# Kernel tuning notes

Measured on AMD Instinct MI355X. Metric: run time of the kernel, lower is better.

The kernel has to match this reference:

```python
import jax, jax.numpy as jnp
import numpy as np

C = 512
H = 8
D = C // H
GROUPS = 32
EPS = 1e-5

def setup_inputs() -> dict:
    key = jax.random.key(0)
    ks = jax.random.split(key, 7)
    B, L = 4, 2048
    x = jax.random.normal(ks[0], (B, C, L), dtype=jnp.float32)
    gamma = jnp.ones((C,), dtype=jnp.float32)
    beta = jnp.zeros((C,), dtype=jnp.float32)
    w_qkv = jax.random.normal(ks[1], (3 * C, C), dtype=jnp.float32) * (1.0 / np.sqrt(C))
    b_qkv = jax.random.normal(ks[2], (3 * C,), dtype=jnp.float32) * 0.01
    w_proj = jax.random.normal(ks[3], (C, C), dtype=jnp.float32) * (1.0 / np.sqrt(C))
    b_proj = jax.random.normal(ks[4], (C,), dtype=jnp.float32) * 0.01
    return {"x": x, "gamma": gamma, "beta": beta, "w_qkv": w_qkv,
            "b_qkv": b_qkv, "w_proj": w_proj, "b_proj": b_proj}

def _group_norm(x, gamma, beta):
    B, Cc, L = x.shape
    xg = x.reshape(B, GROUPS, Cc // GROUPS, L)
    mean = jnp.mean(xg, axis=(2, 3), keepdims=True)
    var = jnp.var(xg, axis=(2, 3), keepdims=True)
    xn = ((xg - mean) * jax.lax.rsqrt(var + EPS)).reshape(B, Cc, L)
    return xn * gamma[None, :, None] + beta[None, :, None]

def reference(x, gamma, beta, w_qkv, b_qkv, w_proj, b_proj):
    B, Cc, L = x.shape
    h = _group_norm(x, gamma, beta)
    # 1x1 conv == channel matmul: (3C,C) x (B,C,L) -> (B,3C,L)
    qkv = jnp.einsum('oc,bcl->bol', w_qkv, h) + b_qkv[None, :, None]
    q, k, v = jnp.split(qkv, 3, axis=1)
    # (B,C,L) -> (B,H,L,D)
    def to_heads(t):
        return t.reshape(B, H, D, L).transpose(0, 1, 3, 2)
    q, k, v = to_heads(q), to_heads(k), to_heads(v)
    scale = 1.0 / np.sqrt(D).astype(np.float32)
    attn = jnp.einsum('bhqd,bhkd->bhqk', q, k) * scale  # [B,H,L,L]
    attn = jax.nn.softmax(attn, axis=-1)
    out = jnp.einsum('bhqk,bhkd->bhqd', attn, v)  # [B,H,L,D]
    out = out.transpose(0, 1, 3, 2).reshape(B, Cc, L)
    proj = jnp.einsum('oc,bcl->bol', w_proj, out) + b_proj[None, :, None]
    return x + proj
```

## Files before the change

kernel.cpp:

```cpp
#include <hip/hip_runtime.h>
#include <stdint.h>

#define C_DIM 512
#define H_HEADS 8
#define D_HEAD 64
#define B_BATCH 4
#define L_SEQ 2048
#define GROUPS 32
#define EPS_GN 1e-5f

typedef unsigned short u16;
typedef __attribute__((ext_vector_type(8))) __bf16 bf16x8;
typedef __attribute__((ext_vector_type(2))) float f32x2;
typedef __attribute__((ext_vector_type(4))) float f32x4;
typedef __attribute__((ext_vector_type(16))) float f32x16;

__device__ __forceinline__ u16 f2bf(float f) {
  unsigned u = __builtin_bit_cast(unsigned, f);
  unsigned r = u + 0x7FFFu + ((u >> 16) & 1u);
  return (u16)(r >> 16);
}

__device__ __forceinline__ unsigned cvtpk_bf16(float lo, float hi) {
  unsigned r;
  asm("v_cvt_pk_bf16_f32 %0, %1, %2" : "=v"(r) : "v"(lo), "v"(hi));
  return r;
}

__device__ __forceinline__ void pl32swap(unsigned& a, unsigned& b) {
  asm("v_permlane32_swap_b32 %0, %1" : "+v"(a), "+v"(b));
}

__device__ __forceinline__ bf16x8 mk8(unsigned a, unsigned b, unsigned c, unsigned d) {
  union { uint4 u; bf16x8 v; } z;
  z.u.x = a; z.u.y = b; z.u.z = c; z.u.w = d;
  return z.v;
}

__device__ __forceinline__ void gl16(const void* g, void* l) {
  __builtin_amdgcn_global_load_lds((const __attribute__((address_space(1))) void*)g,
                                   (__attribute__((address_space(3))) void*)l, 16, 0, 0);
}

__global__ __launch_bounds__(256) void cvt_weights(const float* __restrict__ wq,
                                                   const float* __restrict__ wp,
                                                   u16* __restrict__ wq_bf,
                                                   u16* __restrict__ wp_bf) {
  int i = blockIdx.x * 256 + threadIdx.x;
  const int nq = 3 * C_DIM * C_DIM;
  int idx = i * 4;
  const float* src;
  u16* dst;
  if (idx < nq) { src = wq + idx; dst = wq_bf + idx; }
  else          { src = wp + (idx - nq); dst = wp_bf + (idx - nq); }
  float4 v = *(const float4*)src;
  uint2 pk;
  pk.x = (unsigned)f2bf(v.x) | ((unsigned)f2bf(v.y) << 16);
  pk.y = (unsigned)f2bf(v.z) | ((unsigned)f2bf(v.w) << 16);
  *(uint2*)dst = pk;
}

__global__ __launch_bounds__(256) void groupnorm_kernel(const float* __restrict__ x,
                                                        const float* __restrict__ gamma,
                                                        const float* __restrict__ beta,
                                                        u16* __restrict__ h_t) {
  int bg = blockIdx.x;
  int b = bg >> 5, g = bg & 31;
  const float* base = x + ((size_t)(b * C_DIM + g * 16)) * L_SEQ;
  int t = threadIdx.x;
  int w = t >> 6;
  float s = 0.f, sq = 0.f;
  for (int i = 0; i < 32; ++i) {
    float4 v = ((const float4*)base)[t + i * 256];
    s += v.x + v.y + v.z + v.w;
    sq += v.x * v.x + v.y * v.y + v.z * v.z + v.w * v.w;
  }
  for (int off = 32; off; off >>= 1) { s += __shfl_down(s, off); sq += __shfl_down(sq, off); }
  __shared__ float red[8];
  if ((t & 63) == 0) { red[w * 2] = s; red[w * 2 + 1] = sq; }
  __syncthreads();
  float ts = red[0] + red[2] + red[4] + red[6];
  float tq = red[1] + red[3] + red[5] + red[7];
  float mean = ts * (1.f / 32768.f);
  float var = tq * (1.f / 32768.f) - mean * mean;
  float rstd = rsqrtf(var + EPS_GN);
  float ga[16], be[16];
#pragma unroll
  for (int c = 0; c < 16; ++c) {
    float gm = gamma[g * 16 + c];
    ga[c] = gm * rstd;
    be[c] = beta[g * 16 + c] - mean * gm * rstd;
  }
  __shared__ float tile[16][260];
  for (int lc = 0; lc < 8; ++lc) {
    __syncthreads();
#pragma unroll
    for (int it = 0; it < 4; ++it) {
      int r = it * 4 + w;
      int c4 = (t & 63) * 4;
      *(float4*)&tile[r][c4] = *(const float4*)(base + (size_t)r * L_SEQ + lc * 256 + c4);
    }
    __syncthreads();
    int l = lc * 256 + t;
    unsigned wds[8];
#pragma unroll
    for (int c = 0; c < 8; ++c) {
      float a0 = tile[2 * c][t] * ga[2 * c] + be[2 * c];
      float a1 = tile[2 * c + 1][t] * ga[2 * c + 1] + be[2 * c + 1];
      wds[c] = (unsigned)f2bf(a0) | ((unsigned)f2bf(a1) << 16);
    }
    u16* dst = h_t + ((size_t)(b * L_SEQ + l)) * C_DIM + g * 16;
    uint4 p0; p0.x = wds[0]; p0.y = wds[1]; p0.z = wds[2]; p0.w = wds[3];
    uint4 p1; p1.x = wds[4]; p1.y = wds[5]; p1.z = wds[6]; p1.w = wds[7];
    *(uint4*)dst = p0;
    *(uint4*)(dst + 8) = p1;
  }
}

template <int MODE>
__global__ __launch_bounds__(256) void gemm_kernel(const u16* __restrict__ A_bf,
                                                   const u16* __restrict__ B_t,
                                                   const float* __restrict__ bias,
                                                   const float* __restrict__ xres,
                                                   u16* __restrict__ q_t,
                                                   u16* __restrict__ kf_g,
                                                   u16* __restrict__ vf_g,
                                                   float* __restrict__ out_f) {
  constexpr int K = 512;
  __shared__ u16 A_lds[128][32];
  __shared__ u16 B_lds[128][32];
  int t = threadIdx.x;
  int w = t >> 6, lane = t & 63;
  int q4 = lane >> 4, c15 = lane & 15;
  int wm = w >> 1, wn = w & 1;
  int o0 = blockIdx.y * 128;
  int l0 = blockIdx.x * 128;
  int b = blockIdx.z;
  const u16* Bb = B_t + (size_t)b * L_SEQ * K;
  f32x4 acc[4][4] = {};

  int sr = lane >> 2, sc = lane & 3;
  int r0 = w * 32 + sr;
  int r1 = r0 + 16;
  int lc0 = (sc - (r0 >> 1)) & 3;
  int lc1 = (sc - (r1 >> 1)) & 3;
  const u16* Ag0 = A_bf + (size_t)(o0 + r0) * K + lc0 * 8;
  const u16* Ag1 = A_bf + (size_t)(o0 + r1) * K + lc1 * 8;
  const u16* Bg0 = Bb + (size_t)(l0 + r0) * K + lc0 * 8;
  const u16* Bg1 = Bb + (size_t)(l0 + r1) * K + lc1 * 8;
  u16* Al0 = &A_lds[w * 32][0];
  u16* Al1 = &A_lds[w * 32 + 16][0];
  u16* Bl0 = &B_lds[w * 32][0];
  u16* Bl1 = &B_lds[w * 32 + 16][0];

  for (int kt = 0; kt < K / 32; ++kt) {
    gl16(Ag0, Al0); gl16(Ag1, Al1);
    gl16(Bg0, Bl0); gl16(Bg1, Bl1);
    Ag0 += 32; Ag1 += 32; Bg0 += 32; Bg1 += 32;
    __syncthreads();
    bf16x8 af[4], bfr[4];
#pragma unroll
    for (int mi = 0; mi < 4; ++mi) {
      int ar = wm * 64 + mi * 16 + c15;
      af[mi] = *(const bf16x8*)&A_lds[ar][((q4 + (ar >> 1)) & 3) * 8];
    }
#pragma unroll
    for (int ni = 0; ni < 4; ++ni) {
      int br = wn * 64 + ni * 16 + c15;
      bfr[ni] = *(const bf16x8*)&B_lds[br][((q4 + (br >> 1)) & 3) * 8];
    }
#pragma unroll
    for (int mi = 0; mi < 4; ++mi)
#pragma unroll
      for (int ni = 0; ni < 4; ++ni)
        acc[mi][ni] = __builtin_amdgcn_mfma_f32_16x16x32_bf16(af[mi], bfr[ni], acc[mi][ni], 0, 0, 0);
    __syncthreads();
  }

  if (MODE == 0) {
    const float QS = 0.18033688f;
    int sel = o0 >> 9;
    int ob = o0 - sel * 512 + wm * 64;
#pragma unroll
    for (int mi = 0; mi < 4; ++mi) {
      int orow = ob + mi * 16 + q4 * 4;
      float4 bi = *(const float4*)&bias[o0 + wm * 64 + mi * 16 + q4 * 4];
#pragma unroll
      for (int ni = 0; ni < 4; ++ni) {
        int l = l0 + wn * 64 + ni * 16 + c15;
        float v0 = acc[mi][ni][0] + bi.x;
        float v1 = acc[mi][ni][1] + bi.y;
        float v2 = acc[mi][ni][2] + bi.z;
        float v3 = acc[mi][ni][3] + bi.w;
        if (sel == 0) {
          v0 *= QS; v1 *= QS; v2 *= QS; v3 *= QS;
          uint2 pk;
          pk.x = (unsigned)f2bf(v0) | ((unsigned)f2bf(v1) << 16);
          pk.y = (unsigned)f2bf(v2) | ((unsigned)f2bf(v3) << 16);
          *(uint2*)(q_t + ((size_t)(b * L_SEQ + l)) * C_DIM + orow) = pk;
        } else if (sel == 1) {
          int hh = orow >> 6, d = orow & 63;
          size_t base = ((size_t)(b * 8 + hh)) * 131072 +
                        (size_t)(((l >> 5) * 4 + (d >> 4))) * 512 +
                        (size_t)((l & 31) + ((d >> 3) & 1) * 32) * 8 + (d & 7);
          uint2 pk;
          pk.x = (unsigned)f2bf(v0) | ((unsigned)f2bf(v1) << 16);
          pk.y = (unsigned)f2bf(v2) | ((unsigned)f2bf(v3) << 16);
          *(uint2*)(kf_g + base) = pk;
        } else {
          int hh = orow >> 6, d = orow & 63;
          size_t base0 = ((size_t)(b * 8 + hh)) * 131072 +
                         (size_t)(l >> 4) * 1024 +
                         (size_t)((l >> 3) & 1) * 256 + (l & 7);
          vf_g[base0 + (size_t)((d + 0) >> 5) * 512 + ((d + 0) & 31) * 8] = f2bf(v0);
          vf_g[base0 + (size_t)((d + 1) >> 5) * 512 + ((d + 1) & 31) * 8] = f2bf(v1);
          vf_g[base0 + (size_t)((d + 2) >> 5) * 512 + ((d + 2) & 31) * 8] = f2bf(v2);
          vf_g[base0 + (size_t)((d + 3) >> 5) * 512 + ((d + 3) & 31) * 8] = f2bf(v3);
        }
      }
    }
  } else {
#pragma unroll
    for (int mi = 0; mi < 4; ++mi) {
      int orow = o0 + wm * 64 + mi * 16 + q4 * 4;
      float4 bi = *(const float4*)&bias[orow];
#pragma unroll
      for (int ni = 0; ni < 4; ++ni) {
        int l = l0 + wn * 64 + ni * 16 + c15;
        size_t base2 = ((size_t)(b * C_DIM + orow)) * L_SEQ + l;
        out_f[base2] = acc[mi][ni][0] + bi.x + xres[base2];
        out_f[base2 + L_SEQ] = acc[mi][ni][1] + bi.y + xres[base2 + L_SEQ];
        out_f[base2 + 2 * L_SEQ] = acc[mi][ni][2] + bi.z + xres[base2 + 2 * L_SEQ];
        out_f[base2 + 3 * L_SEQ] = acc[mi][ni][3] + bi.w + xres[base2 + 3 * L_SEQ];
      }
    }
  }
}

#define ATILE(KC, KN, T)                                                       \
  {                                                                            \
    int tn = (T) + 1; tn = tn > 15 ? 15 : tn;                                  \
    const u16* kp = kfb + tn * 2048;                                           \
    const u16* vp = vfb + (T) * 2048;                                          \
    KN[0] = *(const bf16x8*)(kp);                                              \
    KN[1] = *(const bf16x8*)(kp + 512);                                        \
    KN[2] = *(const bf16x8*)(kp + 1024);                                       \
    KN[3] = *(const bf16x8*)(kp + 1536);                                       \
    bf16x8 v0 = *(const bf16x8*)(vp);                                          \
    bf16x8 v1 = *(const bf16x8*)(vp + 512);                                    \
    bf16x8 v2 = *(const bf16x8*)(vp + 1024);                                   \
    bf16x8 v3 = *(const bf16x8*)(vp + 1536);                                   \
    f32x16 s;                                                                  \
    _Pragma("unroll") for (int r = 0; r < 16; ++r) s[r] = 0.f;                 \
    s = __builtin_amdgcn_mfma_f32_32x32x16_bf16(KC[0], qf[0], s, 0, 0, 0);     \
    s = __builtin_amdgcn_mfma_f32_32x32x16_bf16(KC[1], qf[1], s, 0, 0, 0);     \
    s = __builtin_amdgcn_mfma_f32_32x32x16_bf16(KC[2], qf[2], s, 0, 0, 0);     \
    s = __builtin_amdgcn_mfma_f32_32x32x16_bf16(KC[3], qf[3], s, 0, 0, 0);     \
    float mx = fmaxf(fmaxf(s[0], s[1]), s[2]);                                 \
    float m1_ = fmaxf(fmaxf(s[3], s[4]), s[5]);                                \
    float m2_ = fmaxf(fmaxf(s[6], s[7]), s[8]);                                \
    float m3_ = fmaxf(fmaxf(s[9], s[10]), s[11]);                              \
    float m4_ = fmaxf(fmaxf(s[12], s[13]), s[14]);                             \
    mx = fmaxf(fmaxf(mx, s[15]), fmaxf(m1_, m2_));                             \
    mx = fmaxf(mx, fmaxf(m3_, m4_));                                           \
    mx = fmaxf(mx, __shfl_xor(mx, 32));                                        \
    if (__any(mx > m_r + 8.f)) {                                               \
      float mnew = fmaxf(m_r, mx);                                             \
      float al = __builtin_amdgcn_exp2f(m_r - mnew);                           \
      l_r *= al;                                                               \
      _Pragma("unroll") for (int r = 0; r < 16; ++r) { o0[r] *= al; o1[r] *= al; } \
      m_r = mnew;                                                              \
    }                                                                          \
    _Pragma("unroll") for (int r = 0; r < 16; ++r)                             \
        s[r] = __builtin_amdgcn_exp2f(s[r] - m_r);                             \
    f32x2 a0_ = {s[0], s[1]}, a1_ = {s[2], s[3]}, a2_ = {s[4], s[5]},          \
          a3_ = {s[6], s[7]}, a4_ = {s[8], s[9]}, a5_ = {s[10], s[11]},        \
          a6_ = {s[12], s[13]}, a7_ = {s[14], s[15]};                          \
    f32x2 b0_ = a0_ + a1_, b1_ = a2_ + a3_, b2_ = a4_ + a5_, b3_ = a6_ + a7_;  \
    f32x2 c0_ = b0_ + b1_, c1_ = b2_ + b3_;                                    \
    f32x2 d0_ = c0_ + c1_;                                                     \
    float sum = d0_[0] + d0_[1];                                               \
    sum += __shfl_xor(sum, 32);                                                \
    l_r += sum;                                                                \
    unsigned pk[8];                                                            \
    _Pragma("unroll") for (int i = 0; i < 8; ++i)                              \
        pk[i] = cvtpk_bf16(s[2 * i], s[2 * i + 1]);                            \
    pl32swap(pk[0], pk[2]); pl32swap(pk[1], pk[3]);                            \
    pl32swap(pk[4], pk[6]); pl32swap(pk[5], pk[7]);                            \
    bf16x8 pf0 = mk8(pk[0], pk[1], pk[2], pk[3]);                              \
    bf16x8 pf1 = mk8(pk[4], pk[5], pk[6], pk[7]);                              \
    o0 = __builtin_amdgcn_mfma_f32_32x32x16_bf16(v0, pf0, o0, 0, 0, 0);        \
    o1 = __builtin_amdgcn_mfma_f32_32x32x16_bf16(v1, pf0, o1, 0, 0, 0);        \
    o0 = __builtin_amdgcn_mfma_f32_32x32x16_bf16(v2, pf1, o0, 0, 0, 0);        \
    o1 = __builtin_amdgcn_mfma_f32_32x32x16_bf16(v3, pf1, o1, 0, 0, 0);        \
  }

__global__ __launch_bounds__(256, 4) void attn_kernel(const u16* __restrict__ q_t,
                                                      const u16* __restrict__ kf_g,
                                                      const u16* __restrict__ vf_g,
                                                      u16* __restrict__ ao_t) {
  __shared__ float oL[4][64][32];
  __shared__ float mL[4][32];
  __shared__ float lL[4][32];

  int g = blockIdx.x;
  int wk = (g & 7) * 256 + (g >> 3);
  int qg = wk & 63, bh = wk >> 6;
  int b = bh >> 3, h = bh & 7;
  int t = threadIdx.x;
  int wv = t >> 6, lane = t & 63;
  int q = lane & 31, hi = lane >> 5;
  int q0 = qg * 32;

  const u16* qp = q_t + ((size_t)(b * L_SEQ + q0 + q)) * C_DIM + h * 64 + hi * 8;
  bf16x8 qf[4];
#pragma unroll
  for (int kk = 0; kk < 4; ++kk) qf[kk] = *(const bf16x8*)(qp + kk * 16);

  const u16* kfb = kf_g + (size_t)bh * 131072 + (size_t)wv * 32768 + lane * 8;
  const u16* vfb = vf_g + (size_t)bh * 131072 + (size_t)wv * 32768 + lane * 8;

  f32x16 o0, o1;
#pragma unroll
  for (int r = 0; r < 16; ++r) { o0[r] = 0.f; o1[r] = 0.f; }
  float m_r = -1e30f, l_r = 0.f;

  bf16x8 kA[4], kB[4];
#pragma unroll
  for (int i = 0; i < 4; ++i) kA[i] = *(const bf16x8*)(kfb + i * 512);

  for (int it = 0; it < 8; ++it) {
    ATILE(kA, kB, 2 * it);
    ATILE(kB, kA, 2 * it + 1);
  }

  if (hi == 0) mL[wv][q] = m_r;
  __syncthreads();
  float ms = fmaxf(fmaxf(mL[0][q], mL[1][q]), fmaxf(mL[2][q], mL[3][q]));
  float scl = __builtin_amdgcn_exp2f(m_r - ms);
  if (hi == 0) lL[wv][q] = l_r * scl;
#pragma unroll
  for (int r = 0; r < 16; ++r) {
    int d = (r & 3) + 8 * (r >> 2) + 4 * hi;
    oL[wv][d][q] = o0[r] * scl;
    oL[wv][d + 32][q] = o1[r] * scl;
  }
  __syncthreads();

  int tq = t & 31;
  int dbase = (t >> 5) * 8;
  float lsum = (lL[0][tq] + lL[1][tq]) + (lL[2][tq] + lL[3][tq]);
  float inv = 1.f / lsum;
  float v[8];
#pragma unroll
  for (int i = 0; i < 8; ++i) {
    int d = dbase + i;
    v[i] = ((oL[0][d][tq] + oL[1][d][tq]) + (oL[2][d][tq] + oL[3][d][tq])) * inv;
  }
  uint4 ov;
  ov.x = cvtpk_bf16(v[0], v[1]);
  ov.y = cvtpk_bf16(v[2], v[3]);
  ov.z = cvtpk_bf16(v[4], v[5]);
  ov.w = cvtpk_bf16(v[6], v[7]);
  *(uint4*)(ao_t + ((size_t)(b * L_SEQ + q0 + tq)) * C_DIM + h * 64 + dbase) = ov;
}

extern "C" void kernel_launch(void* const* d_in, const int* in_sizes, int n_in,
                              void* d_out, int out_size, void* d_ws, size_t ws_size,
                              hipStream_t stream) {
  const float* x = (const float*)d_in[0];
  const float* gamma = (const float*)d_in[1];
  const float* beta = (const float*)d_in[2];
  const float* w_qkv = (const float*)d_in[3];
  const float* b_qkv = (const float*)d_in[4];
  const float* w_proj = (const float*)d_in[5];
  const float* b_proj = (const float*)d_in[6];
  float* out = (float*)d_out;

  u16* wq_bf = (u16*)d_ws;
  u16* wp_bf = wq_bf + 786432;
  u16* h_t = wp_bf + 262144;
  u16* q_t = h_t + 4194304;
  u16* kf_g = q_t + 4194304;
  u16* vf_g = kf_g + 4194304;
  u16* ao_t = vf_g + 4194304;

  cvt_weights<<<dim3(1024), dim3(256), 0, stream>>>(w_qkv, w_proj, wq_bf, wp_bf);
  groupnorm_kernel<<<dim3(128), dim3(256), 0, stream>>>(x, gamma, beta, h_t);
  gemm_kernel<0><<<dim3(16, 12, 4), dim3(256), 0, stream>>>(wq_bf, h_t, b_qkv, nullptr, q_t, kf_g, vf_g, nullptr);
  attn_kernel<<<dim3(2048), dim3(256), 0, stream>>>(q_t, kf_g, vf_g, ao_t);
  gemm_kernel<1><<<dim3(16, 4, 4), dim3(256), 0, stream>>>(wp_bf, ao_t, b_proj, x, nullptr, nullptr, nullptr, out);
}
```

Before: 112.0 us.

## Fuse weight conversion into groupnorm and split attention into 2 query x 2 KV halves

Merges the weight-conversion and groupnorm kernels into one launch, with extra blocks doing the bf16 conversion. The attention block now covers 64 queries: two query halves each split over two KV halves of 1024 keys, instead of 32 queries over four KV quarters. Each wave processes twice as many key tiles and the final cross-wave reduction combines only two partials, halving the grid. Also switches conversions to packed cvt instructions and vectorizes the row-max reduction with paired max ops. The changes aim to cut launch overhead, repeated Q loads and reduction cost, at the risk of lower parallelism per query and fewer blocks to fill the device.

```diff
diff --git a/kernel.cpp b/kernel.cpp
--- a/kernel.cpp
+++ b/kernel.cpp
@@ -42,28 +42,29 @@
                                    (__attribute__((address_space(3))) void*)l, 16, 0, 0);
 }
 
-__global__ __launch_bounds__(256) void cvt_weights(const float* __restrict__ wq,
+__global__ __launch_bounds__(256) void prep_kernel(const float* __restrict__ x,
+                                                   const float* __restrict__ gamma,
+                                                   const float* __restrict__ beta,
+                                                   const float* __restrict__ wq,
                                                    const float* __restrict__ wp,
+                                                   u16* __restrict__ h_t,
                                                    u16* __restrict__ wq_bf,
                                                    u16* __restrict__ wp_bf) {
-  int i = blockIdx.x * 256 + threadIdx.x;
-  const int nq = 3 * C_DIM * C_DIM;
-  int idx = i * 4;
-  const float* src;
-  u16* dst;
-  if (idx < nq) { src = wq + idx; dst = wq_bf + idx; }
-  else          { src = wp + (idx - nq); dst = wp_bf + (idx - nq); }
-  float4 v = *(const float4*)src;
-  uint2 pk;
-  pk.x = (unsigned)f2bf(v.x) | ((unsigned)f2bf(v.y) << 16);
-  pk.y = (unsigned)f2bf(v.z) | ((unsigned)f2bf(v.w) << 16);
-  *(uint2*)dst = pk;
-}
-
-__global__ __launch_bounds__(256) void groupnorm_kernel(const float* __restrict__ x,
-                                                        const float* __restrict__ gamma,
-                                                        const float* __restrict__ beta,
-                                                        u16* __restrict__ h_t) {
+  if (blockIdx.x >= 128) {
+    int i = (blockIdx.x - 128) * 256 + threadIdx.x;
+    const int nq = 3 * C_DIM * C_DIM;
+    int idx = i * 4;
+    const float* src;
+    u16* dst;
+    if (idx < nq) { src = wq + idx; dst = wq_bf + idx; }
+    else          { src = wp + (idx - nq); dst = wp_bf + (idx - nq); }
+    float4 v = *(const float4*)src;
+    uint2 pk;
+    pk.x = cvtpk_bf16(v.x, v.y);
+    pk.y = cvtpk_bf16(v.z, v.w);
+    *(uint2*)dst = pk;
+    return;
+  }
   int bg = blockIdx.x;
   int b = bg >> 5, g = bg & 31;
   const float* base = x + ((size_t)(b * C_DIM + g * 16)) * L_SEQ;
@@ -107,7 +108,7 @@
     for (int c = 0; c < 8; ++c) {
       float a0 = tile[2 * c][t] * ga[2 * c] + be[2 * c];
       float a1 = tile[2 * c + 1][t] * ga[2 * c + 1] + be[2 * c + 1];
-      wds[c] = (unsigned)f2bf(a0) | ((unsigned)f2bf(a1) << 16);
+      wds[c] = cvtpk_bf16(a0, a1);
     }
     u16* dst = h_t + ((size_t)(b * L_SEQ + l)) * C_DIM + g * 16;
     uint4 p0; p0.x = wds[0]; p0.y = wds[1]; p0.z = wds[2]; p0.w = wds[3];
@@ -195,8 +196,8 @@
         if (sel == 0) {
           v0 *= QS; v1 *= QS; v2 *= QS; v3 *= QS;
           uint2 pk;
-          pk.x = (unsigned)f2bf(v0) | ((unsigned)f2bf(v1) << 16);
-          pk.y = (unsigned)f2bf(v2) | ((unsigned)f2bf(v3) << 16);
+          pk.x = cvtpk_bf16(v0, v1);
+          pk.y = cvtpk_bf16(v2, v3);
           *(uint2*)(q_t + ((size_t)(b * L_SEQ + l)) * C_DIM + orow) = pk;
         } else if (sel == 1) {
           int hh = orow >> 6, d = orow & 63;
@@ -204,8 +205,8 @@
                         (size_t)(((l >> 5) * 4 + (d >> 4))) * 512 +
                         (size_t)((l & 31) + ((d >> 3) & 1) * 32) * 8 + (d & 7);
           uint2 pk;
-          pk.x = (unsigned)f2bf(v0) | ((unsigned)f2bf(v1) << 16);
-          pk.y = (unsigned)f2bf(v2) | ((unsigned)f2bf(v3) << 16);
+          pk.x = cvtpk_bf16(v0, v1);
+          pk.y = cvtpk_bf16(v2, v3);
           *(uint2*)(kf_g + base) = pk;
         } else {
           int hh = orow >> 6, d = orow & 63;
@@ -239,7 +240,7 @@
 
 #define ATILE(KC, KN, T)                                                       \
   {                                                                            \
-    int tn = (T) + 1; tn = tn > 15 ? 15 : tn;                                  \
+    int tn = (T) + 1; tn = tn > 31 ? 31 : tn;                                  \
     const u16* kp = kfb + tn * 2048;                                           \
     const u16* vp = vfb + (T) * 2048;                                          \
     KN[0] = *(const bf16x8*)(kp);                                              \
@@ -256,13 +257,15 @@
     s = __builtin_amdgcn_mfma_f32_32x32x16_bf16(KC[1], qf[1], s, 0, 0, 0);     \
     s = __builtin_amdgcn_mfma_f32_32x32x16_bf16(KC[2], qf[2], s, 0, 0, 0);     \
     s = __builtin_amdgcn_mfma_f32_32x32x16_bf16(KC[3], qf[3], s, 0, 0, 0);     \
-    float mx = fmaxf(fmaxf(s[0], s[1]), s[2]);                                 \
-    float m1_ = fmaxf(fmaxf(s[3], s[4]), s[5]);                                \
-    float m2_ = fmaxf(fmaxf(s[6], s[7]), s[8]);                                \
-    float m3_ = fmaxf(fmaxf(s[9], s[10]), s[11]);                              \
-    float m4_ = fmaxf(fmaxf(s[12], s[13]), s[14]);                             \
-    mx = fmaxf(fmaxf(mx, s[15]), fmaxf(m1_, m2_));                             \
-    mx = fmaxf(mx, fmaxf(m3_, m4_));                                           \
+    f32x2 p0_ = {s[0], s[1]}, p1_ = {s[2], s[3]}, p2_ = {s[4], s[5]},          \
+          p3_ = {s[6], s[7]}, p4_ = {s[8], s[9]}, p5_ = {s[10], s[11]},        \
+          p6_ = {s[12], s[13]}, p7_ = {s[14], s[15]};                          \
+    f32x2 M0 = __builtin_elementwise_max(__builtin_elementwise_max(p0_, p1_),  \
+                                         __builtin_elementwise_max(p2_, p3_)); \
+    f32x2 M1 = __builtin_elementwise_max(__builtin_elementwise_max(p4_, p5_),  \
+                                         __builtin_elementwise_max(p6_, p7_)); \
+    f32x2 M = __builtin_elementwise_max(M0, M1);                               \
+    float mx = fmaxf(M[0], M[1]);                                              \
     mx = fmaxf(mx, __shfl_xor(mx, 32));                                        \
     if (__any(mx > m_r + 8.f)) {                                               \
       float mnew = fmaxf(m_r, mx);                                             \
@@ -304,21 +307,22 @@
   __shared__ float lL[4][32];
 
   int g = blockIdx.x;
-  int wk = (g & 7) * 256 + (g >> 3);
-  int qg = wk & 63, bh = wk >> 6;
+  int wk = (g & 7) * 128 + (g >> 3);
+  int qg = wk & 31, bh = wk >> 5;
   int b = bh >> 3, h = bh & 7;
   int t = threadIdx.x;
   int wv = t >> 6, lane = t & 63;
   int q = lane & 31, hi = lane >> 5;
-  int q0 = qg * 32;
+  int qh = wv & 1, kvh = wv >> 1;
+  int q0 = qg * 64 + qh * 32;
 
   const u16* qp = q_t + ((size_t)(b * L_SEQ + q0 + q)) * C_DIM + h * 64 + hi * 8;
   bf16x8 qf[4];
 #pragma unroll
   for (int kk = 0; kk < 4; ++kk) qf[kk] = *(const bf16x8*)(qp + kk * 16);
 
-  const u16* kfb = kf_g + (size_t)bh * 131072 + (size_t)wv * 32768 + lane * 8;
-  const u16* vfb = vf_g + (size_t)bh * 131072 + (size_t)wv * 32768 + lane * 8;
+  const u16* kfb = kf_g + (size_t)bh * 131072 + (size_t)kvh * 65536 + lane * 8;
+  const u16* vfb = vf_g + (size_t)bh * 131072 + (size_t)kvh * 65536 + lane * 8;
 
   f32x16 o0, o1;
 #pragma unroll
@@ -329,14 +333,14 @@
 #pragma unroll
   for (int i = 0; i < 4; ++i) kA[i] = *(const bf16x8*)(kfb + i * 512);
 
-  for (int it = 0; it < 8; ++it) {
+  for (int it = 0; it < 16; ++it) {
     ATILE(kA, kB, 2 * it);
     ATILE(kB, kA, 2 * it + 1);
   }
 
   if (hi == 0) mL[wv][q] = m_r;
   __syncthreads();
-  float ms = fmaxf(fmaxf(mL[0][q], mL[1][q]), fmaxf(mL[2][q], mL[3][q]));
+  float ms = fmaxf(mL[wv][q], mL[wv ^ 2][q]);
   float scl = __builtin_amdgcn_exp2f(m_r - ms);
   if (hi == 0) lL[wv][q] = l_r * scl;
 #pragma unroll
@@ -348,21 +352,26 @@
   __syncthreads();
 
   int tq = t & 31;
-  int dbase = (t >> 5) * 8;
-  float lsum = (lL[0][tq] + lL[1][tq]) + (lL[2][tq] + lL[3][tq]);
+  int oqh = (t >> 5) & 1;
+  int d0 = (t >> 6) * 16;
+  float lsum = lL[oqh][tq] + lL[oqh + 2][tq];
   float inv = 1.f / lsum;
-  float v[8];
-#pragma unroll
-  for (int i = 0; i < 8; ++i) {
-    int d = dbase + i;
-    v[i] = ((oL[0][d][tq] + oL[1][d][tq]) + (oL[2][d][tq] + oL[3][d][tq])) * inv;
-  }
-  uint4 ov;
-  ov.x = cvtpk_bf16(v[0], v[1]);
-  ov.y = cvtpk_bf16(v[2], v[3]);
-  ov.z = cvtpk_bf16(v[4], v[5]);
-  ov.w = cvtpk_bf16(v[6], v[7]);
-  *(uint4*)(ao_t + ((size_t)(b * L_SEQ + q0 + tq)) * C_DIM + h * 64 + dbase) = ov;
+  float v[16];
+#pragma unroll
+  for (int i = 0; i < 16; ++i)
+    v[i] = (oL[oqh][d0 + i][tq] + oL[oqh + 2][d0 + i][tq]) * inv;
+  u16* dst = ao_t + ((size_t)(b * L_SEQ + qg * 64 + oqh * 32 + tq)) * C_DIM + h * 64 + d0;
+  uint4 ov0, ov1;
+  ov0.x = cvtpk_bf16(v[0], v[1]);
+  ov0.y = cvtpk_bf16(v[2], v[3]);
+  ov0.z = cvtpk_bf16(v[4], v[5]);
+  ov0.w = cvtpk_bf16(v[6], v[7]);
+  ov1.x = cvtpk_bf16(v[8], v[9]);
+  ov1.y = cvtpk_bf16(v[10], v[11]);
+  ov1.z = cvtpk_bf16(v[12], v[13]);
+  ov1.w = cvtpk_bf16(v[14], v[15]);
+  *(uint4*)dst = ov0;
+  *(uint4*)(dst + 8) = ov1;
 }
 
 extern "C" void kernel_launch(void* const* d_in, const int* in_sizes, int n_in,
@@ -385,9 +394,9 @@
   u16* vf_g = kf_g + 4194304;
   u16* ao_t = vf_g + 4194304;
 
-  cvt_weights<<<dim3(1024), dim3(256), 0, stream>>>(w_qkv, w_proj, wq_bf, wp_bf);
-  groupnorm_kernel<<<dim3(128), dim3(256), 0, stream>>>(x, gamma, beta, h_t);
+  prep_kernel<<<dim3(1152), dim3(256), 0, stream>>>(x, gamma, beta, w_qkv, w_proj,
+                                                    h_t, wq_bf, wp_bf);
   gemm_kernel<0><<<dim3(16, 12, 4), dim3(256), 0, stream>>>(wq_bf, h_t, b_qkv, nullptr, q_t, kf_g, vf_g, nullptr);
-  attn_kernel<<<dim3(2048), dim3(256), 0, stream>>>(q_t, kf_g, vf_g, ao_t);
+  attn_kernel<<<dim3(1024), dim3(256), 0, stream>>>(q_t, kf_g, vf_g, ao_t);
   gemm_kernel<1><<<dim3(16, 4, 4), dim3(256), 0, stream>>>(wp_bf, ao_t, b_proj, x, nullptr, nullptr, nullptr, out);
 }
```

New measurement: 105.9 us. 5.4% less time.
